# Kernel tuning notes

Hardware: AMD Instinct MI355X
Metric: run time of the kernel (lower is better)

## Reference

```python
import jax, jax.numpy as jnp
import numpy as np

N_NODES = 50000
N_EDGES = 800000
IN_FEATS = 128
OUT_FEATS = 128


def mean_agg(feat, src, dst, num_nodes):
    # DGL copy_u + mean reduce: mean of in-neighbor (src) features per dst node;
    # nodes with zero in-degree get 0.
    msg = feat[src]                                        # [E, D] gather
    summed = jax.ops.segment_sum(msg, dst, num_segments=num_nodes)  # [N, D]
    deg = jax.ops.segment_sum(jnp.ones((src.shape[0],), feat.dtype), dst,
                              num_segments=num_nodes)      # [N]
    return summed / jnp.maximum(deg, 1.0)[:, None]


def setup_inputs() -> dict:
    key = jax.random.key(0)
    ks = jax.random.split(key, 16)
    sx = 1.0 / np.sqrt(IN_FEATS)
    sh = 1.0 / np.sqrt(OUT_FEATS)
    inp = {
        "x": jax.random.normal(ks[0], (N_NODES, IN_FEATS), jnp.float32),
        "h": jax.random.normal(ks[1], (N_NODES, OUT_FEATS), jnp.float32),
        "c": jax.random.normal(ks[2], (N_NODES, OUT_FEATS), jnp.float32),
        # stacked weights for the 4 gates (order: i, f, c, o)
        "Wx_self": jax.random.normal(ks[3], (4, IN_FEATS, OUT_FEATS), jnp.float32) * sx,
        "Wx_neigh": jax.random.normal(ks[4], (4, IN_FEATS, OUT_FEATS), jnp.float32) * sx,
        "Wh_self": jax.random.normal(ks[5], (4, OUT_FEATS, OUT_FEATS), jnp.float32) * sh,
        "Wh_neigh": jax.random.normal(ks[6], (4, OUT_FEATS, OUT_FEATS), jnp.float32) * sh,
        "w_ci": jax.random.uniform(ks[7], (OUT_FEATS,), jnp.float32),
        "w_cf": jax.random.uniform(ks[8], (OUT_FEATS,), jnp.float32),
        "w_co": jax.random.uniform(ks[9], (OUT_FEATS,), jnp.float32),
        "b_i": jax.random.uniform(ks[10], (OUT_FEATS,), jnp.float32),
        "b_f": jax.random.uniform(ks[11], (OUT_FEATS,), jnp.float32),
        "b_c": jax.random.uniform(ks[12], (OUT_FEATS,), jnp.float32),
        "b_o": jax.random.uniform(ks[13], (OUT_FEATS,), jnp.float32),
        "src": jax.random.randint(ks[14], (N_EDGES,), 0, N_NODES, jnp.int32),
        "dst": jax.random.randint(ks[15], (N_EDGES,), 0, N_NODES, jnp.int32),
    }
    return inp


def reference(x, h, c, Wx_self, Wx_neigh, Wh_self, Wh_neigh,
              w_ci, w_cf, w_co, b_i, b_f, b_c, b_o, src, dst):
    n = x.shape[0]
    # reuse_gate_rz=True: compute the two mean-aggregations once, shared by all nets
    h_N = mean_agg(x, src, dst, n)      # neighbor mean of x  [N, in]
    h_agg = mean_agg(h, src, dst, n)    # neighbor mean of h  [N, out]

    # each sub-net: net(g, feat, h_N=agg) = feat @ W_self + agg @ W_neigh
    # batched over the 4 gates (i, f, c, o)
    gx = jnp.einsum('ni,gio->gno', x, Wx_self) + jnp.einsum('ni,gio->gno', h_N, Wx_neigh)
    gh = jnp.einsum('no,goe->gne', h, Wh_self) + jnp.einsum('no,goe->gne', h_agg, Wh_neigh)
    s = gx + gh                          # [4, N, out]

    i = jax.nn.sigmoid(s[0] + w_ci * c + b_i)
    f = jax.nn.sigmoid(s[1] + w_cf * c + b_f)
    c_tilde = jnp.tanh(s[2] + b_c)
    new_c = f * c + i * c_tilde
    o = jax.nn.sigmoid(s[3] + w_co * new_c + b_o)
    new_h = o * jnp.tanh(new_c)
    return new_h, new_c
```

## Files before the change

kernel.cpp:

```cpp
#include <hip/hip_runtime.h>
#include <hip/hip_bf16.h>
#include <stdint.h>

#define N_NODES 50000
#define N_EDGES 800000
#define D 128
#define NPAD 50048
#define HKD 256
#define KDIM 512

typedef __attribute__((ext_vector_type(8))) __bf16 bf16x8;
typedef __attribute__((ext_vector_type(4))) __bf16 bf16x4;
typedef __attribute__((ext_vector_type(4))) float f32x4;

__device__ __forceinline__ void gload_lds16(const void* g, void* l) {
  __builtin_amdgcn_global_load_lds(
      (const __attribute__((address_space(1))) unsigned int*)(uintptr_t)g,
      (__attribute__((address_space(3))) unsigned int*)(uint32_t)(uintptr_t)l,
      16, 0, 0);
}

__device__ __forceinline__ float sigm(float v) { return 1.0f / (1.0f + __expf(-v)); }
__device__ __forceinline__ float tanh_fast(float v) { return 1.0f - 2.0f / (1.0f + __expf(2.0f * v)); }

#define NB_DEG 3125
#define NB_TOB 6250
#define NB_PKW 1024
__global__ void k_pre(const int* __restrict__ dst, int* __restrict__ deg,
                      const float* __restrict__ x, const float* __restrict__ h,
                      __bf16* __restrict__ XH,
                      const float* __restrict__ Wx_self, const float* __restrict__ Wx_neigh,
                      const float* __restrict__ Wh_self, const float* __restrict__ Wh_neigh,
                      __bf16* __restrict__ Wp) {
  int b = blockIdx.x;
  if (b < NB_DEG) {
    int e = b * 256 + threadIdx.x;
    atomicAdd(&deg[dst[e]], 1);
  } else if (b < NB_DEG + NB_TOB) {
    int idx = (b - NB_DEG) * 256 + threadIdx.x;
    int node = idx >> 5;
    int f4 = (idx & 31) << 2;
    float4 xv = *(const float4*)(x + (size_t)node * D + f4);
    float4 hv = *(const float4*)(h + (size_t)node * D + f4);
    bf16x4 a, bb;
    a[0] = (__bf16)xv.x; a[1] = (__bf16)xv.y; a[2] = (__bf16)xv.z; a[3] = (__bf16)xv.w;
    bb[0] = (__bf16)hv.x; bb[1] = (__bf16)hv.y; bb[2] = (__bf16)hv.z; bb[3] = (__bf16)hv.w;
    __bf16* xhrow = XH + (size_t)node * HKD;
    *(bf16x4*)(xhrow + f4) = a;
    *(bf16x4*)(xhrow + 128 + f4) = bb;
  } else {
    int idx = (b - NB_DEG - NB_TOB) * 256 + threadIdx.x;
    int e = idx & 7;
    int r16 = (idx >> 3) & 15;
    int q = (idx >> 7) & 3;
    int s = (idx >> 9) & 15;
    int G = idx >> 13;
    int wrow = G * 16 + r16;
    int g = wrow >> 7, o = wrow & 127;
    int k = s * 32 + q * 8 + e;
    const float* src; int i;
    if (k < 128)      { src = Wx_self;  i = k; }
    else if (k < 256) { src = Wh_self;  i = k - 128; }
    else if (k < 384) { src = Wx_neigh; i = k - 256; }
    else              { src = Wh_neigh; i = k - 384; }
    Wp[idx] = (__bf16)src[(g << 14) + (i << 7) + o];
  }
}

__global__ __launch_bounds__(1024) void k_scan(const int* __restrict__ deg, int* __restrict__ offs,
                                               int* __restrict__ cursor, int n) {
  const int t = threadIdx.x;
  const int lane = t & 63;
  const int w = t >> 6;
  __shared__ int wsum[16];
  __shared__ int carry_s;
  int carry = 0;
  for (int base = 0; base < n; base += 4096) {
    int idx = base + t * 4;
    int4 v = make_int4(0, 0, 0, 0);
    if (idx < n) v = *(const int4*)(deg + idx);
    int tsum = v.x + v.y + v.z + v.w;
    int s = tsum;
#pragma unroll
    for (int d = 1; d < 64; d <<= 1) {
      int u = __shfl_up(s, d, 64);
      if (lane >= d) s += u;
    }
    if (lane == 63) wsum[w] = s;
    __syncthreads();
    int woff = 0;
    for (int i = 0; i < w; i++) woff += wsum[i];
    int excl = carry + woff + (s - tsum);
    if (idx < n) {
      int4 o;
      o.x = excl; o.y = excl + v.x; o.z = o.y + v.y; o.w = o.z + v.z;
      *(int4*)(offs + idx) = o;
      *(int4*)(cursor + idx) = o;
    }
    __syncthreads();
    if (t == 0) {
      int tot = carry;
#pragma unroll
      for (int i = 0; i < 16; i++) tot += wsum[i];
      carry_s = tot;
    }
    __syncthreads();
    carry = carry_s;
  }
  if (t == 0) offs[n] = carry;
}

__global__ void k_fill(const int* __restrict__ src, const int* __restrict__ dst,
                       int* __restrict__ cursor, int* __restrict__ bins) {
  int e = blockIdx.x * 256 + threadIdx.x;
  if (e < N_EDGES) {
    int d = dst[e];
    int p = atomicAdd(&cursor[d], 1);
    bins[p] = src[e];
  }
}

__global__ void k_gather(const int* __restrict__ offs, const int* __restrict__ bins,
                         const __bf16* __restrict__ XH, __bf16* __restrict__ ZM) {
  int wid = (blockIdx.x * 256 + threadIdx.x) >> 6;
  int lane = threadIdx.x & 63;
  if (wid >= NPAD) return;
  if (wid >= N_NODES) {
    ((uint2*)(XH + (size_t)wid * HKD))[lane] = make_uint2(0, 0);
    ((uint2*)(ZM + (size_t)wid * HKD))[lane] = make_uint2(0, 0);
    return;
  }
  const int half = lane >> 5;
  const int li = lane & 31;
  const int srcoff = li * 8;
  int beg = offs[wid], end = offs[wid + 1];
  float a[8] = {0.f, 0.f, 0.f, 0.f, 0.f, 0.f, 0.f, 0.f};
  float a2[8] = {0.f, 0.f, 0.f, 0.f, 0.f, 0.f, 0.f, 0.f};
  int j = beg + half;
  for (; j + 2 < end; j += 4) {
    int s0 = bins[j];
    int s1 = bins[j + 2];
    bf16x8 v0 = *(const bf16x8*)(XH + (size_t)s0 * HKD + srcoff);
    bf16x8 v1 = *(const bf16x8*)(XH + (size_t)s1 * HKD + srcoff);
#pragma unroll
    for (int e = 0; e < 8; ++e) { a[e] += (float)v0[e]; a2[e] += (float)v1[e]; }
  }
  if (j < end) {
    int s0 = bins[j];
    bf16x8 v0 = *(const bf16x8*)(XH + (size_t)s0 * HKD + srcoff);
#pragma unroll
    for (int e = 0; e < 8; ++e) a[e] += (float)v0[e];
  }
#pragma unroll
  for (int e = 0; e < 8; ++e) {
    a[e] += a2[e];
    a[e] += __shfl_xor(a[e], 32, 64);
  }
  int degn = end - beg;
  float inv = 1.0f / (float)(degn > 0 ? degn : 1);
  if (lane < 32) {
    bf16x8 bb;
#pragma unroll
    for (int e = 0; e < 8; ++e) bb[e] = (__bf16)(a[e] * inv);
    *(bf16x8*)(ZM + (size_t)wid * HKD + srcoff) = bb;
  }
}

__global__ __launch_bounds__(512, 4) void k_gemm(
    const __bf16* __restrict__ XH, const __bf16* __restrict__ ZM, const __bf16* __restrict__ Wp,
    const float* __restrict__ c,
    const float* __restrict__ w_ci, const float* __restrict__ w_cf, const float* __restrict__ w_co,
    const float* __restrict__ b_i, const float* __restrict__ b_f, const float* __restrict__ b_c,
    const float* __restrict__ b_o,
    float* __restrict__ out_h, float* __restrict__ out_c) {
  __shared__ __align__(16) __bf16 As[64 * KDIM];
  const int t = threadIdx.x;
  const int lane = t & 63;
  const int w = t >> 6;
  const int m0 = blockIdx.x * 64;
  const int l15 = lane & 15;
  const int q = lane >> 4;

#pragma unroll
  for (int i = 0; i < 8; ++i) {
    int s = i * 512 + t;
    int row = s >> 6;
    int cg = (s & 63) ^ (row & 7);
    const __bf16* src = (cg < 32) ? (XH + (size_t)(m0 + row) * HKD + cg * 8)
                                  : (ZM + (size_t)(m0 + row) * HKD + (cg - 32) * 8);
    gload_lds16(src, (__bf16*)As + s * 8);
  }
  __syncthreads();

  f32x4 acc[4][4];
#pragma unroll
  for (int m = 0; m < 4; ++m)
#pragma unroll
    for (int g = 0; g < 4; ++g) acc[m][g] = (f32x4){0.f, 0.f, 0.f, 0.f};

  const __bf16* wp = Wp + (size_t)(w * 16) * 512 + lane * 8;

  bf16x8 bA[4], bB[4];
#pragma unroll
  for (int g = 0; g < 4; ++g) bA[g] = *(const bf16x8*)(wp + g * 65536);

#pragma unroll
  for (int s2 = 0; s2 < 8; ++s2) {
    {
      const int step = 2 * s2;
#pragma unroll
      for (int g = 0; g < 4; ++g)
        bB[g] = *(const bf16x8*)(wp + g * 65536 + (step + 1) * 512);
      bf16x8 af[4];
#pragma unroll
      for (int m = 0; m < 4; ++m) {
        int row = m * 16 + l15;
        int cl = (step * 4 + q) ^ (row & 7);
        af[m] = *(const bf16x8*)(As + (row * 64 + cl) * 8);
      }
#pragma unroll
      for (int m = 0; m < 4; ++m)
#pragma unroll
        for (int g = 0; g < 4; ++g)
          acc[m][g] = __builtin_amdgcn_mfma_f32_16x16x32_bf16(af[m], bA[g], acc[m][g], 0, 0, 0);
    }
    {
      const int step = 2 * s2 + 1;
      if (step < 15) {
#pragma unroll
        for (int g = 0; g < 4; ++g)
          bA[g] = *(const bf16x8*)(wp + g * 65536 + (step + 1) * 512);
      }
      bf16x8 af[4];
#pragma unroll
      for (int m = 0; m < 4; ++m) {
        int row = m * 16 + l15;
        int cl = (step * 4 + q) ^ (row & 7);
        af[m] = *(const bf16x8*)(As + (row * 64 + cl) * 8);
      }
#pragma unroll
      for (int m = 0; m < 4; ++m)
#pragma unroll
        for (int g = 0; g < 4; ++g)
          acc[m][g] = __builtin_amdgcn_mfma_f32_16x16x32_bf16(af[m], bB[g], acc[m][g], 0, 0, 0);
    }
  }

  const int o = w * 16 + l15;
  const float wci = w_ci[o], wcf = w_cf[o], wco = w_co[o];
  const float bi = b_i[o], bfv = b_f[o], bc = b_c[o], bo = b_o[o];
#pragma unroll
  for (int m = 0; m < 4; ++m) {
#pragma unroll
    for (int r = 0; r < 4; ++r) {
      int row = m0 + m * 16 + q * 4 + r;
      if (row < N_NODES) {
        float cv = c[(size_t)row * D + o];
        float ig = sigm(acc[m][0][r] + wci * cv + bi);
        float fg = sigm(acc[m][1][r] + wcf * cv + bfv);
        float ct = tanh_fast(acc[m][2][r] + bc);
        float nc = fg * cv + ig * ct;
        float og = sigm(acc[m][3][r] + wco * nc + bo);
        out_h[(size_t)row * D + o] = og * tanh_fast(nc);
        out_c[(size_t)row * D + o] = nc;
      }
    }
  }
}

extern "C" void kernel_launch(void* const* d_in, const int* in_sizes, int n_in,
                              void* d_out, int out_size, void* d_ws, size_t ws_size,
                              hipStream_t stream) {
  const float* x = (const float*)d_in[0];
  const float* h = (const float*)d_in[1];
  const float* c = (const float*)d_in[2];
  const float* Wx_self = (const float*)d_in[3];
  const float* Wx_neigh = (const float*)d_in[4];
  const float* Wh_self = (const float*)d_in[5];
  const float* Wh_neigh = (const float*)d_in[6];
  const float* w_ci = (const float*)d_in[7];
  const float* w_cf = (const float*)d_in[8];
  const float* w_co = (const float*)d_in[9];
  const float* b_i = (const float*)d_in[10];
  const float* b_f = (const float*)d_in[11];
  const float* b_c = (const float*)d_in[12];
  const float* b_o = (const float*)d_in[13];
  const int* src = (const int*)d_in[14];
  const int* dst = (const int*)d_in[15];

  char* ws = (char*)d_ws;
  int* deg = (int*)(ws);
  int* offs = (int*)(ws + 200704);
  int* cursor = (int*)(ws + 400896);
  int* bins = (int*)(ws + 601088);
  __bf16* XH = (__bf16*)(ws + 4194304);
  __bf16* ZM = (__bf16*)(ws + 29818880);
  __bf16* Wp = (__bf16*)(ws + 55443456);

  float* out_h = (float*)d_out;
  float* out_c = out_h + (size_t)N_NODES * D;

  hipMemsetAsync(deg, 0, N_NODES * sizeof(int), stream);
  k_pre<<<NB_DEG + NB_TOB + NB_PKW, 256, 0, stream>>>(dst, deg, x, h, XH,
                                                      Wx_self, Wx_neigh, Wh_self, Wh_neigh, Wp);
  k_scan<<<1, 1024, 0, stream>>>(deg, offs, cursor, N_NODES);
  k_fill<<<(N_EDGES + 255) / 256, 256, 0, stream>>>(src, dst, cursor, bins);
  k_gather<<<NPAD / 4, 256, 0, stream>>>(offs, bins, XH, ZM);
  k_gemm<<<NPAD / 64, 512, 0, stream>>>(XH, ZM, Wp, c, w_ci, w_cf, w_co,
                                        b_i, b_f, b_c, b_o, out_h, out_c);
}
```

Before: 229.2 us.

## Store gather source features in FP8 and load self features directly in GEMM

The gather source table of x and h now uses FP8 e4m3 instead of bf16, which halves the bytes fetched per random neighbor read in the aggregation kernel. The gather loop is unrolled to four outstanding loads per half-wave. The GEMM now reads the self features as fp32 straight from x and h and converts them to bf16 into LDS, so it no longer depends on the bf16 copy. MFMA sections are also wrapped in s_setprio. The cost is lower precision in the neighbor means, since FP8 e4m3 has only 3 mantissa bits, which risks tolerance failures.

```diff
diff --git a/kernel.cpp b/kernel.cpp
--- a/kernel.cpp
+++ b/kernel.cpp
@@ -12,6 +12,7 @@
 typedef __attribute__((ext_vector_type(8))) __bf16 bf16x8;
 typedef __attribute__((ext_vector_type(4))) __bf16 bf16x4;
 typedef __attribute__((ext_vector_type(4))) float f32x4;
+typedef __attribute__((ext_vector_type(2))) float f32x2;
 
 __device__ __forceinline__ void gload_lds16(const void* g, void* l) {
   __builtin_amdgcn_global_load_lds(
@@ -23,12 +24,33 @@
 __device__ __forceinline__ float sigm(float v) { return 1.0f / (1.0f + __expf(-v)); }
 __device__ __forceinline__ float tanh_fast(float v) { return 1.0f - 2.0f / (1.0f + __expf(2.0f * v)); }
 
+#if defined(__has_builtin) && __has_builtin(__builtin_amdgcn_cvt_pk_fp8_f32) && __has_builtin(__builtin_amdgcn_cvt_pk_f32_fp8)
+__device__ __forceinline__ unsigned pack_fp8x4(float a, float b, float c, float d) {
+  int p = __builtin_amdgcn_cvt_pk_fp8_f32(a, b, 0, false);
+  p = __builtin_amdgcn_cvt_pk_fp8_f32(c, d, p, true);
+  return (unsigned)p;
+}
+__device__ __forceinline__ f32x2 unpk_fp8_lo(unsigned u) { return __builtin_amdgcn_cvt_pk_f32_fp8(u, false); }
+__device__ __forceinline__ f32x2 unpk_fp8_hi(unsigned u) { return __builtin_amdgcn_cvt_pk_f32_fp8(u, true); }
+#else
+#include <hip/hip_fp8.h>
+__device__ __forceinline__ unsigned pack_fp8x4(float a, float b, float c, float d) {
+  __hip_fp8_e4m3 qa(a), qb(b), qc(c), qd(d);
+  return (unsigned)qa.__x | ((unsigned)qb.__x << 8) | ((unsigned)qc.__x << 16) | ((unsigned)qd.__x << 24);
+}
+__device__ __forceinline__ float unpk1(unsigned byte) {
+  __hip_fp8_e4m3 t; t.__x = (__hip_fp8_storage_t)byte; return (float)t;
+}
+__device__ __forceinline__ f32x2 unpk_fp8_lo(unsigned u) { f32x2 r; r.x = unpk1(u & 0xff); r.y = unpk1((u >> 8) & 0xff); return r; }
+__device__ __forceinline__ f32x2 unpk_fp8_hi(unsigned u) { f32x2 r; r.x = unpk1((u >> 16) & 0xff); r.y = unpk1(u >> 24); return r; }
+#endif
+
 #define NB_DEG 3125
 #define NB_TOB 6250
 #define NB_PKW 1024
 __global__ void k_pre(const int* __restrict__ dst, int* __restrict__ deg,
                       const float* __restrict__ x, const float* __restrict__ h,
-                      __bf16* __restrict__ XH,
+                      uint8_t* __restrict__ XH8,
                       const float* __restrict__ Wx_self, const float* __restrict__ Wx_neigh,
                       const float* __restrict__ Wh_self, const float* __restrict__ Wh_neigh,
                       __bf16* __restrict__ Wp) {
@@ -42,12 +64,9 @@
     int f4 = (idx & 31) << 2;
     float4 xv = *(const float4*)(x + (size_t)node * D + f4);
     float4 hv = *(const float4*)(h + (size_t)node * D + f4);
-    bf16x4 a, bb;
-    a[0] = (__bf16)xv.x; a[1] = (__bf16)xv.y; a[2] = (__bf16)xv.z; a[3] = (__bf16)xv.w;
-    bb[0] = (__bf16)hv.x; bb[1] = (__bf16)hv.y; bb[2] = (__bf16)hv.z; bb[3] = (__bf16)hv.w;
-    __bf16* xhrow = XH + (size_t)node * HKD;
-    *(bf16x4*)(xhrow + f4) = a;
-    *(bf16x4*)(xhrow + 128 + f4) = bb;
+    uint8_t* r = XH8 + (size_t)node * HKD;
+    *(unsigned*)(r + f4) = pack_fp8x4(xv.x, xv.y, xv.z, xv.w);
+    *(unsigned*)(r + 128 + f4) = pack_fp8x4(hv.x, hv.y, hv.z, hv.w);
   } else {
     int idx = (b - NB_DEG - NB_TOB) * 256 + threadIdx.x;
     int e = idx & 7;
@@ -121,59 +140,60 @@
 }
 
 __global__ void k_gather(const int* __restrict__ offs, const int* __restrict__ bins,
-                         const __bf16* __restrict__ XH, __bf16* __restrict__ ZM) {
+                         const uint8_t* __restrict__ XH8, __bf16* __restrict__ ZM) {
   int wid = (blockIdx.x * 256 + threadIdx.x) >> 6;
   int lane = threadIdx.x & 63;
   if (wid >= NPAD) return;
   if (wid >= N_NODES) {
-    ((uint2*)(XH + (size_t)wid * HKD))[lane] = make_uint2(0, 0);
     ((uint2*)(ZM + (size_t)wid * HKD))[lane] = make_uint2(0, 0);
     return;
   }
   const int half = lane >> 5;
   const int li = lane & 31;
-  const int srcoff = li * 8;
+  const int boff = li * 8;
   int beg = offs[wid], end = offs[wid + 1];
   float a[8] = {0.f, 0.f, 0.f, 0.f, 0.f, 0.f, 0.f, 0.f};
-  float a2[8] = {0.f, 0.f, 0.f, 0.f, 0.f, 0.f, 0.f, 0.f};
+  auto acc = [&](uint2 v) {
+    f32x2 p;
+    p = unpk_fp8_lo(v.x); a[0] += p.x; a[1] += p.y;
+    p = unpk_fp8_hi(v.x); a[2] += p.x; a[3] += p.y;
+    p = unpk_fp8_lo(v.y); a[4] += p.x; a[5] += p.y;
+    p = unpk_fp8_hi(v.y); a[6] += p.x; a[7] += p.y;
+  };
   int j = beg + half;
-  for (; j + 2 < end; j += 4) {
-    int s0 = bins[j];
-    int s1 = bins[j + 2];
-    bf16x8 v0 = *(const bf16x8*)(XH + (size_t)s0 * HKD + srcoff);
-    bf16x8 v1 = *(const bf16x8*)(XH + (size_t)s1 * HKD + srcoff);
-#pragma unroll
-    for (int e = 0; e < 8; ++e) { a[e] += (float)v0[e]; a2[e] += (float)v1[e]; }
-  }
-  if (j < end) {
-    int s0 = bins[j];
-    bf16x8 v0 = *(const bf16x8*)(XH + (size_t)s0 * HKD + srcoff);
-#pragma unroll
-    for (int e = 0; e < 8; ++e) a[e] += (float)v0[e];
-  }
-#pragma unroll
-  for (int e = 0; e < 8; ++e) {
-    a[e] += a2[e];
-    a[e] += __shfl_xor(a[e], 32, 64);
-  }
+  for (; j + 6 < end; j += 8) {
+    int s0 = bins[j], s1 = bins[j + 2], s2 = bins[j + 4], s3 = bins[j + 6];
+    uint2 v0 = *(const uint2*)(XH8 + (size_t)s0 * HKD + boff);
+    uint2 v1 = *(const uint2*)(XH8 + (size_t)s1 * HKD + boff);
+    uint2 v2 = *(const uint2*)(XH8 + (size_t)s2 * HKD + boff);
+    uint2 v3 = *(const uint2*)(XH8 + (size_t)s3 * HKD + boff);
+    acc(v0); acc(v1); acc(v2); acc(v3);
+  }
+  for (; j < end; j += 2) {
+    uint2 v = *(const uint2*)(XH8 + (size_t)bins[j] * HKD + boff);
+    acc(v);
+  }
+#pragma unroll
+  for (int e = 0; e < 8; ++e) a[e] += __shfl_xor(a[e], 32, 64);
   int degn = end - beg;
   float inv = 1.0f / (float)(degn > 0 ? degn : 1);
   if (lane < 32) {
     bf16x8 bb;
 #pragma unroll
     for (int e = 0; e < 8; ++e) bb[e] = (__bf16)(a[e] * inv);
-    *(bf16x8*)(ZM + (size_t)wid * HKD + srcoff) = bb;
+    *(bf16x8*)(ZM + (size_t)wid * HKD + boff) = bb;
   }
 }
 
 __global__ __launch_bounds__(512, 4) void k_gemm(
-    const __bf16* __restrict__ XH, const __bf16* __restrict__ ZM, const __bf16* __restrict__ Wp,
+    const float* __restrict__ xg, const float* __restrict__ hg,
+    const __bf16* __restrict__ ZM, const __bf16* __restrict__ Wp,
     const float* __restrict__ c,
     const float* __restrict__ w_ci, const float* __restrict__ w_cf, const float* __restrict__ w_co,
     const float* __restrict__ b_i, const float* __restrict__ b_f, const float* __restrict__ b_c,
     const float* __restrict__ b_o,
     float* __restrict__ out_h, float* __restrict__ out_c) {
-  __shared__ __align__(16) __bf16 As[64 * KDIM];
+  __shared__ __align__(16) __bf16 As[4096 * 8];
   const int t = threadIdx.x;
   const int lane = t & 63;
   const int w = t >> 6;
@@ -182,13 +202,30 @@
   const int q = lane >> 4;
 
 #pragma unroll
-  for (int i = 0; i < 8; ++i) {
-    int s = i * 512 + t;
-    int row = s >> 6;
-    int cg = (s & 63) ^ (row & 7);
-    const __bf16* src = (cg < 32) ? (XH + (size_t)(m0 + row) * HKD + cg * 8)
-                                  : (ZM + (size_t)(m0 + row) * HKD + (cg - 32) * 8);
-    gload_lds16(src, (__bf16*)As + s * 8);
+  for (int i = 0; i < 4; ++i) {
+    int u = i * 512 + t;
+    int row = u >> 5, cz = u & 31;
+    int cg = cz ^ (row & 7);
+    gload_lds16(ZM + (size_t)(m0 + row) * HKD + cg * 8, (__bf16*)As + (2048 + u) * 8);
+  }
+#pragma unroll
+  for (int i = 0; i < 4; ++i) {
+    int u = i * 512 + t;
+    int row = u >> 5, cs = u & 31;
+    int slot = row * 32 + (cs ^ (row & 7));
+    int grow = m0 + row;
+    bf16x8 val;
+#pragma unroll
+    for (int e = 0; e < 8; ++e) val[e] = (__bf16)0.f;
+    if (grow < N_NODES) {
+      const float* sp = (cs < 16) ? (xg + (size_t)grow * D + cs * 8)
+                                  : (hg + (size_t)grow * D + (cs - 16) * 8);
+      float4 u0 = *(const float4*)sp;
+      float4 u1 = *(const float4*)(sp + 4);
+      val[0] = (__bf16)u0.x; val[1] = (__bf16)u0.y; val[2] = (__bf16)u0.z; val[3] = (__bf16)u0.w;
+      val[4] = (__bf16)u1.x; val[5] = (__bf16)u1.y; val[6] = (__bf16)u1.z; val[7] = (__bf16)u1.w;
+    }
+    *(bf16x8*)((__bf16*)As + slot * 8) = val;
   }
   __syncthreads();
 
@@ -199,6 +236,16 @@
     for (int g = 0; g < 4; ++g) acc[m][g] = (f32x4){0.f, 0.f, 0.f, 0.f};
 
   const __bf16* wp = Wp + (size_t)(w * 16) * 512 + lane * 8;
+
+  auto LOADA = [&](int step, bf16x8* af) {
+    const int base = (step < 8) ? 0 : 2048;
+    const int cq = ((step < 8) ? step * 4 : (step - 8) * 4) + q;
+#pragma unroll
+    for (int m = 0; m < 4; ++m) {
+      int row = m * 16 + l15;
+      af[m] = *(const bf16x8*)((__bf16*)As + (base + row * 32 + (cq ^ (row & 7))) * 8);
+    }
+  };
 
   bf16x8 bA[4], bB[4];
 #pragma unroll
@@ -212,17 +259,14 @@
       for (int g = 0; g < 4; ++g)
         bB[g] = *(const bf16x8*)(wp + g * 65536 + (step + 1) * 512);
       bf16x8 af[4];
-#pragma unroll
-      for (int m = 0; m < 4; ++m) {
-        int row = m * 16 + l15;
-        int cl = (step * 4 + q) ^ (row & 7);
-        af[m] = *(const bf16x8*)(As + (row * 64 + cl) * 8);
-      }
+      LOADA(step, af);
+      __builtin_amdgcn_s_setprio(1);
 #pragma unroll
       for (int m = 0; m < 4; ++m)
 #pragma unroll
         for (int g = 0; g < 4; ++g)
           acc[m][g] = __builtin_amdgcn_mfma_f32_16x16x32_bf16(af[m], bA[g], acc[m][g], 0, 0, 0);
+      __builtin_amdgcn_s_setprio(0);
     }
     {
       const int step = 2 * s2 + 1;
@@ -232,17 +276,14 @@
           bA[g] = *(const bf16x8*)(wp + g * 65536 + (step + 1) * 512);
       }
       bf16x8 af[4];
-#pragma unroll
-      for (int m = 0; m < 4; ++m) {
-        int row = m * 16 + l15;
-        int cl = (step * 4 + q) ^ (row & 7);
-        af[m] = *(const bf16x8*)(As + (row * 64 + cl) * 8);
-      }
+      LOADA(step, af);
+      __builtin_amdgcn_s_setprio(1);
 #pragma unroll
       for (int m = 0; m < 4; ++m)
 #pragma unroll
         for (int g = 0; g < 4; ++g)
           acc[m][g] = __builtin_amdgcn_mfma_f32_16x16x32_bf16(af[m], bB[g], acc[m][g], 0, 0, 0);
+      __builtin_amdgcn_s_setprio(0);
     }
   }
 
@@ -293,19 +334,19 @@
   int* offs = (int*)(ws + 200704);
   int* cursor = (int*)(ws + 400896);
   int* bins = (int*)(ws + 601088);
-  __bf16* XH = (__bf16*)(ws + 4194304);
-  __bf16* ZM = (__bf16*)(ws + 29818880);
-  __bf16* Wp = (__bf16*)(ws + 55443456);
+  uint8_t* XH8 = (uint8_t*)(ws + 4194304);
+  __bf16* ZM = (__bf16*)(ws + 17039360);
+  __bf16* Wp = (__bf16*)(ws + 42729472);
 
   float* out_h = (float*)d_out;
   float* out_c = out_h + (size_t)N_NODES * D;
 
   hipMemsetAsync(deg, 0, N_NODES * sizeof(int), stream);
-  k_pre<<<NB_DEG + NB_TOB + NB_PKW, 256, 0, stream>>>(dst, deg, x, h, XH,
+  k_pre<<<NB_DEG + NB_TOB + NB_PKW, 256, 0, stream>>>(dst, deg, x, h, XH8,
                                                       Wx_self, Wx_neigh, Wh_self, Wh_neigh, Wp);
   k_scan<<<1, 1024, 0, stream>>>(deg, offs, cursor, N_NODES);
   k_fill<<<(N_EDGES + 255) / 256, 256, 0, stream>>>(src, dst, cursor, bins);
-  k_gather<<<NPAD / 4, 256, 0, stream>>>(offs, bins, XH, ZM);
-  k_gemm<<<NPAD / 64, 512, 0, stream>>>(XH, ZM, Wp, c, w_ci, w_cf, w_co,
+  k_gather<<<NPAD / 4, 256, 0, stream>>>(offs, bins, XH8, ZM);
+  k_gemm<<<NPAD / 64, 512, 0, stream>>>(x, h, ZM, Wp, c, w_ci, w_cf, w_co,
                                         b_i, b_f, b_c, b_o, out_h, out_c);
 }
```

Result: faster. 219.1 us (-4.4%).
